# Optimization experiments

Measured on AMD Instinct MI355X. Metric: run time of the kernel, lower is better.

Reference implementation:

```python
import jax, jax.numpy as jnp
import numpy as np


def setup_inputs() -> dict:
    key = jax.random.key(0)
    ks = jax.random.split(key, 8)
    B, Te, De, Dd, H = 64, 1024, 1024, 1024, 1024
    return {
        "encoder_outputs": jax.random.normal(ks[0], (B, Te, De), jnp.float32),
        "decoder_outputs": jax.random.normal(ks[1], (B, 1, Dd), jnp.float32),
        "Wa_w": jax.random.normal(ks[2], (H, Dd), jnp.float32) * 0.02,
        "Wa_b": jax.random.normal(ks[3], (H,), jnp.float32) * 0.02,
        "Ua_w": jax.random.normal(ks[4], (H, De), jnp.float32) * 0.02,
        "Ua_b": jax.random.normal(ks[5], (H,), jnp.float32) * 0.02,
        "Va_w": jax.random.normal(ks[6], (1, H), jnp.float32) * 0.02,
        "Va_b": jax.random.normal(ks[7], (1,), jnp.float32) * 0.02,
    }


def reference(encoder_outputs, decoder_outputs, Wa_w, Wa_b, Ua_w, Ua_b, Va_w, Va_b):
    # Wa: [B,1,H], Ua: [B,Te,H]  (torch Linear: x @ W.T + b)
    Wa = jnp.einsum('bqd,hd->bqh', decoder_outputs, Wa_w) + Wa_b
    Ua = jnp.einsum('bed,hd->beh', encoder_outputs, Ua_w) + Ua_b
    # broadcast add -> tanh -> scalar score per encoder position: [B,Te,1]
    scores = jnp.einsum('beh,oh->beo', jnp.tanh(Wa + Ua), Va_w) + Va_b
    scores = jnp.transpose(scores, (0, 2, 1))          # [B,1,Te]
    weights = jax.nn.softmax(scores, axis=-1)          # softmax over Te
    context = jnp.einsum('bqe,bed->bqd', weights, encoder_outputs)  # [B,1,De]
    return context
```

## Files before the change

kernel.cpp:

```cpp
#include <hip/hip_runtime.h>
#include <hip/hip_bf16.h>

#define B_  64
#define TE  1024
#define K_  1024
#define HH  1024
#define MM  (B_ * TE)

typedef __bf16 bf16x8 __attribute__((ext_vector_type(8)));
typedef __bf16 bf16x4 __attribute__((ext_vector_type(4)));
typedef float  f32x4  __attribute__((ext_vector_type(4)));

__device__ __forceinline__ float fast_tanh(float x) {
    float ax = __builtin_fabsf(x);
    float t  = __expf(-2.0f * ax);
    float r  = (1.0f - t) * __builtin_amdgcn_rcpf(1.0f + t);
    return __builtin_copysignf(r, x);
}

__global__ __launch_bounds__(256) void prep_kernel(const float* __restrict__ Ua_w,
                                                   __bf16* __restrict__ uawB,
                                                   const float* __restrict__ dec,
                                                   const float* __restrict__ Wa_w,
                                                   const float* __restrict__ Wa_b,
                                                   float* __restrict__ WaOut) {
    int bid = blockIdx.x, tid = threadIdx.x;
    if (bid < 256) {
        const long n4 = (long)HH * 1024 / 4;
        const float4* in4 = (const float4*)Ua_w;
        bf16x4* out4 = (bf16x4*)uawB;
        for (long j = bid * 256 + tid; j < n4; j += 65536) {
            float4 v = in4[j];
            bf16x4 o;
            o[0] = (__bf16)v.x; o[1] = (__bf16)v.y; o[2] = (__bf16)v.z; o[3] = (__bf16)v.w;
            out4[j] = o;
        }
        return;
    }
    int wb = bid - 256;
    int b = wb >> 4, hc = wb & 15;
    int wave = tid >> 6, lane = tid & 63;

    const float4* d4 = (const float4*)(dec + b * 1024);
    float4 dreg[4];
    #pragma unroll
    for (int j = 0; j < 4; j++) dreg[j] = d4[lane * 4 + j];

    #pragma unroll 4
    for (int i = 0; i < 16; i++) {
        int h = hc * 64 + wave * 16 + i;
        const float4* wr = (const float4*)(Wa_w + (long)h * 1024);
        float a = 0.0f;
        #pragma unroll
        for (int j = 0; j < 4; j++) {
            float4 v = wr[lane * 4 + j];
            a += v.x * dreg[j].x + v.y * dreg[j].y + v.z * dreg[j].z + v.w * dreg[j].w;
        }
        #pragma unroll
        for (int off = 32; off > 0; off >>= 1)
            a += __shfl_xor(a, off, 64);
        if (lane == 0) WaOut[b * 1024 + h] = a + Wa_b[h];
    }
}

#define MT 128
#define NP 128
#define KT 64

__global__ __launch_bounds__(256, 3) void score_gemm(
    const float* __restrict__ Af,
    __bf16* __restrict__ encB,
    const __bf16* __restrict__ Bm,
    const float* __restrict__ Wa,
    const float* __restrict__ Ua_b,
    const float* __restrict__ Va_w,
    float* __restrict__ scores)
{
    __shared__ __bf16 sA[MT * KT];
    __shared__ __bf16 sB[NP * KT];
    __shared__ float sVa[NP];
    __shared__ float sWU[NP];

    const int tid  = threadIdx.x;
    const int wave = tid >> 6;
    const int lane = tid & 63;
    const int quad = lane >> 4;
    const int l16  = lane & 15;
    const int wm   = wave >> 1;
    const int wn   = wave & 1;

    const int bid = blockIdx.x;
    const int grp = bid >> 6;
    const int r6  = bid & 63;
    const int y   = r6 >> 3;
    const int x   = grp * 8 + (r6 & 7);

    const int rowBase = x * MT;
    const int colBase = y * NP;
    const int b       = rowBase >> 10;
    const bool wb     = (y == 0);

    if (tid < NP) {
        int h = colBase + tid;
        sVa[tid] = Va_w[h];
        sWU[tid] = Wa[b * 1024 + h] + Ua_b[h];
    }

    int rr[4], sg[4];
    #pragma unroll
    for (int i = 0; i < 4; i++) {
        int c = i * 256 + tid;
        rr[i] = c >> 3;
        sg[i] = (c & 7) ^ (rr[i] & 7);
    }

    f32x4 acc[4][4] = {};

    const long aBase = (long)rowBase * K_;
    const long bBase = (long)colBase * K_;

    float4 pre[4][2];
    #pragma unroll
    for (int i = 0; i < 4; i++) {
        const float4* p = (const float4*)(Af + aBase + (long)rr[i] * K_ + sg[i] * 8);
        pre[i][0] = p[0]; pre[i][1] = p[1];
    }

    for (int k0 = 0; k0 < K_; k0 += KT) {
        __syncthreads();
        #pragma unroll
        for (int i = 0; i < 4; i++) {
            int c = i * 256 + tid;
            int r = c >> 3, slot = c & 7;
            int seg = slot ^ (r & 7);
            __builtin_amdgcn_global_load_lds(
                (const __attribute__((address_space(1))) unsigned int*)(Bm + bBase + (long)r * K_ + k0 + seg * 8),
                (__attribute__((address_space(3))) unsigned int*)(sB + c * 8), 16, 0, 0);
        }
        #pragma unroll
        for (int i = 0; i < 4; i++) {
            bf16x8 v;
            v[0] = (__bf16)pre[i][0].x; v[1] = (__bf16)pre[i][0].y;
            v[2] = (__bf16)pre[i][0].z; v[3] = (__bf16)pre[i][0].w;
            v[4] = (__bf16)pre[i][1].x; v[5] = (__bf16)pre[i][1].y;
            v[6] = (__bf16)pre[i][1].z; v[7] = (__bf16)pre[i][1].w;
            *(bf16x8*)(sA + (i * 256 + tid) * 8) = v;
            if (wb)
                *(bf16x8*)(encB + aBase + (long)rr[i] * K_ + k0 + sg[i] * 8) = v;
        }
        __syncthreads();

        if (k0 + KT < K_) {
            #pragma unroll
            for (int i = 0; i < 4; i++) {
                const float4* p = (const float4*)(Af + aBase + (long)rr[i] * K_ + (k0 + KT) + sg[i] * 8);
                pre[i][0] = p[0]; pre[i][1] = p[1];
            }
        }

        #pragma unroll
        for (int ks = 0; ks < 2; ks++) {
            bf16x8 bfr[4];
            #pragma unroll
            for (int t = 0; t < 4; t++) {
                int r = wn * 64 + t * 16 + l16;
                int slot = (ks * 4 + quad) ^ (r & 7);
                bfr[t] = *(const bf16x8*)(sB + r * KT + slot * 8);
            }
            #pragma unroll
            for (int s = 0; s < 4; s++) {
                int r = wm * 64 + s * 16 + l16;
                int slot = (ks * 4 + quad) ^ (r & 7);
                bf16x8 af = *(const bf16x8*)(sA + r * KT + slot * 8);
                #pragma unroll
                for (int t = 0; t < 4; t++)
                    acc[s][t] = __builtin_amdgcn_mfma_f32_16x16x32_bf16(af, bfr[t], acc[s][t], 0, 0, 0);
            }
        }
    }

    float rs[4][4] = {};
    #pragma unroll
    for (int s = 0; s < 4; s++)
        #pragma unroll
        for (int t = 0; t < 4; t++) {
            int hl = wn * 64 + t * 16 + l16;
            float va = sVa[hl], wu = sWU[hl];
            #pragma unroll
            for (int r = 0; r < 4; r++)
                rs[s][r] += va * fast_tanh(acc[s][t][r] + wu);
        }

    #pragma unroll
    for (int s = 0; s < 4; s++)
        #pragma unroll
        for (int r = 0; r < 4; r++) {
            float v = rs[s][r];
            v += __shfl_xor(v, 1, 64);
            v += __shfl_xor(v, 2, 64);
            v += __shfl_xor(v, 4, 64);
            v += __shfl_xor(v, 8, 64);
            if (l16 == 0)
                atomicAdd(&scores[rowBase + wm * 64 + s * 16 + quad * 4 + r], v);
        }
}

__global__ __launch_bounds__(256) void softmax_kernel(float* __restrict__ s) {
    __shared__ float red[8];
    int b = blockIdx.x, tid = threadIdx.x;
    int wave = tid >> 6, lane = tid & 63;
    float4* row = (float4*)(s + b * 1024);
    float4 v = row[tid];
    float m = fmaxf(fmaxf(v.x, v.y), fmaxf(v.z, v.w));
    #pragma unroll
    for (int off = 32; off > 0; off >>= 1)
        m = fmaxf(m, __shfl_xor(m, off, 64));
    if (lane == 0) red[wave] = m;
    __syncthreads();
    m = fmaxf(fmaxf(red[0], red[1]), fmaxf(red[2], red[3]));
    v.x = expf(v.x - m); v.y = expf(v.y - m); v.z = expf(v.z - m); v.w = expf(v.w - m);
    float sum = v.x + v.y + v.z + v.w;
    #pragma unroll
    for (int off = 32; off > 0; off >>= 1)
        sum += __shfl_xor(sum, off, 64);
    if (lane == 0) red[4 + wave] = sum;
    __syncthreads();
    float inv = 1.0f / (red[4] + red[5] + red[6] + red[7]);
    v.x *= inv; v.y *= inv; v.z *= inv; v.w *= inv;
    row[tid] = v;
}

__global__ __launch_bounds__(256) void context_partial(const __bf16* __restrict__ enc,
                                                       const float* __restrict__ w,
                                                       float* __restrict__ pb) {
    __shared__ float red[2][128][8];
    int b = blockIdx.x, ec = blockIdx.y, tid = threadIdx.x;
    int eo = tid >> 7;
    int dc = tid & 127;
    const bf16x8* enc8 = (const bf16x8*)(enc + ((long)b * 1024 + ec * 128) * 1024);
    const float* wrow = w + b * 1024 + ec * 128;
    float acc[8] = {};
    #pragma unroll 4
    for (int e = eo; e < 128; e += 2) {
        float we = wrow[e];
        bf16x8 v = enc8[e * 128 + dc];
        #pragma unroll
        for (int j = 0; j < 8; j++) acc[j] += we * (float)v[j];
    }
    #pragma unroll
    for (int j = 0; j < 8; j++) red[eo][dc][j] = acc[j];
    __syncthreads();
    if (eo == 0) {
        float* o = pb + ((long)(b * 8 + ec)) * 1024 + dc * 8;
        #pragma unroll
        for (int j = 0; j < 8; j++) o[j] = red[0][dc][j] + red[1][dc][j];
    }
}

__global__ void context_reduce(const float* __restrict__ pb, float* __restrict__ out) {
    int b = blockIdx.x, tid = threadIdx.x;
    const f32x4* p4 = (const f32x4*)pb;
    f32x4 s = {0.f, 0.f, 0.f, 0.f};
    #pragma unroll
    for (int ec = 0; ec < 8; ec++)
        s += p4[(b * 8 + ec) * 256 + tid];
    ((f32x4*)out)[b * 256 + tid] = s;
}

extern "C" void kernel_launch(void* const* d_in, const int* in_sizes, int n_in,
                              void* d_out, int out_size, void* d_ws, size_t ws_size,
                              hipStream_t stream) {
    (void)in_sizes; (void)n_in; (void)ws_size;
    const float* enc   = (const float*)d_in[0];
    const float* dec   = (const float*)d_in[1];
    const float* Wa_w  = (const float*)d_in[2];
    const float* Wa_b  = (const float*)d_in[3];
    const float* Ua_w  = (const float*)d_in[4];
    const float* Ua_b  = (const float*)d_in[5];
    const float* Va_w  = (const float*)d_in[6];
    float* out = (float*)d_out;

    char* w = (char*)d_ws;
    __bf16* encB = (__bf16*)w;  w += (size_t)MM * 1024 * 2;
    __bf16* uawB = (__bf16*)w;  w += (size_t)HH * 1024 * 2;
    float* WaBuf = (float*)w;   w += (size_t)B_ * HH * 4;
    float* scores = (float*)w;  w += (size_t)MM * 4;
    float* pb = (float*)w;      w += (size_t)B_ * 8 * 1024 * 4;

    hipMemsetAsync(scores, 0, (size_t)MM * 4, stream);
    prep_kernel<<<dim3(256 + B_ * 16), 256, 0, stream>>>(Ua_w, uawB, dec, Wa_w, Wa_b, WaBuf);
    score_gemm<<<dim3((MM / MT) * (HH / NP)), 256, 0, stream>>>(enc, encB, uawB, WaBuf, Ua_b, Va_w, scores);
    softmax_kernel<<<dim3(B_), 256, 0, stream>>>(scores);
    context_partial<<<dim3(B_, 8), 256, 0, stream>>>(encB, scores, pb);
    context_reduce<<<dim3(B_), 256, 0, stream>>>(pb, out);
}
```

Measured before the change: 563.7 us.

## Widen score GEMM N tile to 256, fuse softmax into context, fold memset

Doubles the score GEMM column tile from 128 to 256, with each wave computing 64x128 outputs. This halves how many times the fp32 encoder tile is re-read and converted to bf16 across H blocks, at the cost of twice the accumulator registers and lower occupancy (launch bounds 3 to 2). The softmax kernel is removed: each context_partial block recomputes the row max and sum and stages its normalized weights in LDS. The scores memset moves into prep_kernel, and the B-tile async loads are now issued after the A-tile stores.

Result: faster. 511.2 us (-9.3%).

```diff
diff --git a/kernel.cpp b/kernel.cpp
--- a/kernel.cpp
+++ b/kernel.cpp
@@ -23,9 +23,12 @@
                                                    const float* __restrict__ dec,
                                                    const float* __restrict__ Wa_w,
                                                    const float* __restrict__ Wa_b,
-                                                   float* __restrict__ WaOut) {
+                                                   float* __restrict__ WaOut,
+                                                   float* __restrict__ scores) {
     int bid = blockIdx.x, tid = threadIdx.x;
     if (bid < 256) {
+        long zi = (long)bid * 256 + tid;
+        if (zi < MM / 4) ((f32x4*)scores)[zi] = f32x4{0.f, 0.f, 0.f, 0.f};
         const long n4 = (long)HH * 1024 / 4;
         const float4* in4 = (const float4*)Ua_w;
         bf16x4* out4 = (bf16x4*)uawB;
@@ -64,10 +67,10 @@
 }
 
 #define MT 128
-#define NP 128
+#define NP 256
 #define KT 64
 
-__global__ __launch_bounds__(256, 3) void score_gemm(
+__global__ __launch_bounds__(256, 2) void score_gemm(
     const float* __restrict__ Af,
     __bf16* __restrict__ encB,
     const __bf16* __restrict__ Bm,
@@ -90,10 +93,10 @@
     const int wn   = wave & 1;
 
     const int bid = blockIdx.x;
-    const int grp = bid >> 6;
-    const int r6  = bid & 63;
-    const int y   = r6 >> 3;
-    const int x   = grp * 8 + (r6 & 7);
+    const int grp = bid >> 5;
+    const int r5  = bid & 31;
+    const int y   = r5 >> 3;
+    const int x   = grp * 8 + (r5 & 7);
 
     const int rowBase = x * MT;
     const int colBase = y * NP;
@@ -114,7 +117,7 @@
         sg[i] = (c & 7) ^ (rr[i] & 7);
     }
 
-    f32x4 acc[4][4] = {};
+    f32x4 acc[4][8] = {};
 
     const long aBase = (long)rowBase * K_;
     const long bBase = (long)colBase * K_;
@@ -128,15 +131,6 @@
 
     for (int k0 = 0; k0 < K_; k0 += KT) {
         __syncthreads();
-        #pragma unroll
-        for (int i = 0; i < 4; i++) {
-            int c = i * 256 + tid;
-            int r = c >> 3, slot = c & 7;
-            int seg = slot ^ (r & 7);
-            __builtin_amdgcn_global_load_lds(
-                (const __attribute__((address_space(1))) unsigned int*)(Bm + bBase + (long)r * K_ + k0 + seg * 8),
-                (__attribute__((address_space(3))) unsigned int*)(sB + c * 8), 16, 0, 0);
-        }
         #pragma unroll
         for (int i = 0; i < 4; i++) {
             bf16x8 v;
@@ -148,6 +142,15 @@
             if (wb)
                 *(bf16x8*)(encB + aBase + (long)rr[i] * K_ + k0 + sg[i] * 8) = v;
         }
+        #pragma unroll
+        for (int i = 0; i < 8; i++) {
+            int c = i * 256 + tid;
+            int r = c >> 3, slot = c & 7;
+            int seg = slot ^ (r & 7);
+            __builtin_amdgcn_global_load_lds(
+                (const __attribute__((address_space(1))) unsigned int*)(Bm + bBase + (long)r * K_ + k0 + seg * 8),
+                (__attribute__((address_space(3))) unsigned int*)(sB + c * 8), 16, 0, 0);
+        }
         __syncthreads();
 
         if (k0 + KT < K_) {
@@ -160,10 +163,10 @@
 
         #pragma unroll
         for (int ks = 0; ks < 2; ks++) {
-            bf16x8 bfr[4];
+            bf16x8 bfr[8];
             #pragma unroll
-            for (int t = 0; t < 4; t++) {
-                int r = wn * 64 + t * 16 + l16;
+            for (int t = 0; t < 8; t++) {
+                int r = wn * 128 + t * 16 + l16;
                 int slot = (ks * 4 + quad) ^ (r & 7);
                 bfr[t] = *(const bf16x8*)(sB + r * KT + slot * 8);
             }
@@ -173,7 +176,7 @@
                 int slot = (ks * 4 + quad) ^ (r & 7);
                 bf16x8 af = *(const bf16x8*)(sA + r * KT + slot * 8);
                 #pragma unroll
-                for (int t = 0; t < 4; t++)
+                for (int t = 0; t < 8; t++)
                     acc[s][t] = __builtin_amdgcn_mfma_f32_16x16x32_bf16(af, bfr[t], acc[s][t], 0, 0, 0);
             }
         }
@@ -183,8 +186,8 @@
     #pragma unroll
     for (int s = 0; s < 4; s++)
         #pragma unroll
-        for (int t = 0; t < 4; t++) {
-            int hl = wn * 64 + t * 16 + l16;
+        for (int t = 0; t < 8; t++) {
+            int hl = wn * 128 + t * 16 + l16;
             float va = sVa[hl], wu = sWU[hl];
             #pragma unroll
             for (int r = 0; r < 4; r++)
@@ -205,47 +208,50 @@
         }
 }
 
-__global__ __launch_bounds__(256) void softmax_kernel(float* __restrict__ s) {
-    __shared__ float red[8];
-    int b = blockIdx.x, tid = threadIdx.x;
+__global__ __launch_bounds__(256) void context_partial(const __bf16* __restrict__ enc,
+                                                       const float* __restrict__ sc,
+                                                       float* __restrict__ pb) {
+    __shared__ float red[2][128][8];
+    __shared__ float wLds[128];
+    __shared__ float xr[8];
+    int b = blockIdx.x, ec = blockIdx.y, tid = threadIdx.x;
     int wave = tid >> 6, lane = tid & 63;
-    float4* row = (float4*)(s + b * 1024);
-    float4 v = row[tid];
+
+    float4 v = ((const float4*)(sc + b * 1024))[tid];
     float m = fmaxf(fmaxf(v.x, v.y), fmaxf(v.z, v.w));
     #pragma unroll
     for (int off = 32; off > 0; off >>= 1)
         m = fmaxf(m, __shfl_xor(m, off, 64));
-    if (lane == 0) red[wave] = m;
+    if (lane == 0) xr[wave] = m;
     __syncthreads();
-    m = fmaxf(fmaxf(red[0], red[1]), fmaxf(red[2], red[3]));
-    v.x = expf(v.x - m); v.y = expf(v.y - m); v.z = expf(v.z - m); v.w = expf(v.w - m);
-    float sum = v.x + v.y + v.z + v.w;
+    m = fmaxf(fmaxf(xr[0], xr[1]), fmaxf(xr[2], xr[3]));
+    float ex = expf(v.x - m), ey = expf(v.y - m), ez = expf(v.z - m), ew = expf(v.w - m);
+    float sum = ex + ey + ez + ew;
     #pragma unroll
     for (int off = 32; off > 0; off >>= 1)
         sum += __shfl_xor(sum, off, 64);
-    if (lane == 0) red[4 + wave] = sum;
+    if (lane == 0) xr[4 + wave] = sum;
     __syncthreads();
-    float inv = 1.0f / (red[4] + red[5] + red[6] + red[7]);
-    v.x *= inv; v.y *= inv; v.z *= inv; v.w *= inv;
-    row[tid] = v;
-}
-
-__global__ __launch_bounds__(256) void context_partial(const __bf16* __restrict__ enc,
-                                                       const float* __restrict__ w,
-                                                       float* __restrict__ pb) {
-    __shared__ float red[2][128][8];
-    int b = blockIdx.x, ec = blockIdx.y, tid = threadIdx.x;
+    float inv = 1.0f / (xr[4] + xr[5] + xr[6] + xr[7]);
+    int u = tid - ec * 32;
+    if (u >= 0 && u < 32) {
+        wLds[u * 4 + 0] = ex * inv;
+        wLds[u * 4 + 1] = ey * inv;
+        wLds[u * 4 + 2] = ez * inv;
+        wLds[u * 4 + 3] = ew * inv;
+    }
+    __syncthreads();
+
     int eo = tid >> 7;
     int dc = tid & 127;
     const bf16x8* enc8 = (const bf16x8*)(enc + ((long)b * 1024 + ec * 128) * 1024);
-    const float* wrow = w + b * 1024 + ec * 128;
     float acc[8] = {};
     #pragma unroll 4
     for (int e = eo; e < 128; e += 2) {
-        float we = wrow[e];
-        bf16x8 v = enc8[e * 128 + dc];
-        #pragma unroll
-        for (int j = 0; j < 8; j++) acc[j] += we * (float)v[j];
+        float we = wLds[e];
+        bf16x8 vv = enc8[e * 128 + dc];
+        #pragma unroll
+        for (int j = 0; j < 8; j++) acc[j] += we * (float)vv[j];
     }
     #pragma unroll
     for (int j = 0; j < 8; j++) red[eo][dc][j] = acc[j];
@@ -270,7 +276,7 @@
 extern "C" void kernel_launch(void* const* d_in, const int* in_sizes, int n_in,
                               void* d_out, int out_size, void* d_ws, size_t ws_size,
                               hipStream_t stream) {
-    (void)in_sizes; (void)n_in; (void)ws_size;
+    (void)in_sizes; (void)n_in; (void)ws_size; (void)out_size;
     const float* enc   = (const float*)d_in[0];
     const float* dec   = (const float*)d_in[1];
     const float* Wa_w  = (const float*)d_in[2];
@@ -287,10 +293,8 @@
     float* scores = (float*)w;  w += (size_t)MM * 4;
     float* pb = (float*)w;      w += (size_t)B_ * 8 * 1024 * 4;
 
-    hipMemsetAsync(scores, 0, (size_t)MM * 4, stream);
-    prep_kernel<<<dim3(256 + B_ * 16), 256, 0, stream>>>(Ua_w, uawB, dec, Wa_w, Wa_b, WaBuf);
+    prep_kernel<<<dim3(256 + B_ * 16), 256, 0, stream>>>(Ua_w, uawB, dec, Wa_w, Wa_b, WaBuf, scores);
     score_gemm<<<dim3((MM / MT) * (HH / NP)), 256, 0, stream>>>(enc, encB, uawB, WaBuf, Ua_b, Va_w, scores);
-    softmax_kernel<<<dim3(B_), 256, 0, stream>>>(scores);
     context_partial<<<dim3(B_, 8), 256, 0, stream>>>(encB, scores, pb);
     context_reduce<<<dim3(B_), 256, 0, stream>>>(pb, out);
 }
```
